# Optimization experiments

Hardware: AMD Instinct MI355X
Metric: run time of the kernel (lower is better)

## Reference

```python
import jax, jax.numpy as jnp
import numpy as np

NUM_SAMPLES = 9


def _resize1d(x, out_size, axis):
    """Bilinear (align_corners=False) resize along one axis, matching torch."""
    in_size = x.shape[axis]
    scale = in_size / out_size
    dst = jnp.arange(out_size, dtype=jnp.float32)
    src = jnp.maximum((dst + 0.5) * scale - 0.5, 0.0)
    i0 = jnp.floor(src).astype(jnp.int32)
    w1 = (src - i0).astype(x.dtype)
    i0 = jnp.clip(i0, 0, in_size - 1)
    i1 = jnp.clip(i0 + 1, 0, in_size - 1)
    x0 = jnp.take(x, i0, axis=axis)
    x1 = jnp.take(x, i1, axis=axis)
    wshape = [1] * x.ndim
    wshape[axis] = out_size
    w1 = w1.reshape(wshape)
    return x0 * (1.0 - w1) + x1 * w1


def _rel_to_abs(x, ns):
    # x: (b, h, l, ns+l-1) -> (b, h, l, ns) via the pad/reshape skew trick
    b, h, l, c = x.shape
    x = jnp.pad(x, ((0, 0), (0, 0), (0, 0), (0, 1)))
    x = x.reshape(b, h, l * (c + 1))
    x = jnp.pad(x, ((0, 0), (0, 0), (0, ns - 1)))
    x = x.reshape(b, h, l + 1, ns + l - 1)
    return x[:, :, :l, l - 1:]


def _relative_logits_1d(q, rel_k, ns):
    # q: (b, heads, x, y, d); rel_k: (y+ns-1, d)
    logits = jnp.einsum('bhxyd,rd->bhxyr', q, rel_k)
    b, h, x, y, r = logits.shape
    logits = logits.reshape(b, h * x, y, r)
    return _rel_to_abs(logits, ns)


def setup_inputs() -> dict:
    key = jax.random.key(0)
    k1, k2, k3 = jax.random.split(key, 3)
    B, heads, Hh, Ww, d = 16, 8, 64, 64, 64
    scale = d ** (-0.5)
    q = jax.random.normal(k1, (B, heads, Hh, Ww, d), dtype=jnp.float32)
    rel_height = jax.random.normal(k2, (Hh + NUM_SAMPLES - 1, d), dtype=jnp.float32) * scale
    rel_width = jax.random.normal(k3, (Ww + NUM_SAMPLES - 1, d), dtype=jnp.float32) * scale
    return {"q": q, "H": Hh, "W": Ww, "rel_height": rel_height, "rel_width": rel_width}


def reference(q, H, W, rel_height, rel_width):
    ns = NUM_SAMPLES
    heads = q.shape[1]
    # bilinear resize of learned tables along the positional axis
    # (the dim_head axis is resized to its own size -> identity)
    rel_w = _resize1d(rel_width, W + ns - 1, axis=0)
    rel_h = _resize1d(rel_height, H + ns - 1, axis=0)

    rel_logits_w = _relative_logits_1d(q, rel_w, ns)          # (b, heads*H, W, ns)
    qT = jnp.swapaxes(q, 2, 3)                                # (b, heads, W, H, d)
    rel_logits_h = _relative_logits_1d(qT, rel_h, ns)         # (b, heads*W, H, ns)

    # torch interpolates (b, ns, heads*W, H) -> (heads*H, W); separable bilinear
    rel_logits_h = _resize1d(rel_logits_h, heads * H, axis=1)
    rel_logits_h = _resize1d(rel_logits_h, W, axis=2)
    return rel_logits_w + rel_logits_h
```

## Files before the change

### kernel.cpp

```cpp
#include <hip/hip_runtime.h>
#include <stdint.h>

#define NS 9

typedef _Float16 f16x8 __attribute__((ext_vector_type(8)));
typedef float    f32x4 __attribute__((ext_vector_type(4)));

#define SBAR __builtin_amdgcn_sched_barrier(0)
#define WAIT_VM(N) do { SBAR; asm volatile("s_waitcnt vmcnt(" #N ")" ::: "memory"); SBAR; } while (0)
#define WAIT_LGKM0 do { SBAR; asm volatile("s_waitcnt lgkmcnt(0)" ::: "memory"); SBAR; } while (0)

__device__ __forceinline__ unsigned int pk(float a, float b) {
    return __builtin_bit_cast(unsigned int, __builtin_amdgcn_cvt_pkrtz(a, b));
}


__global__ __launch_bounds__(256, 2) void relpos_kernel(
    const float* __restrict__ q,
    const float* __restrict__ relh,
    const float* __restrict__ relw,
    float* __restrict__ out)
{
    __shared__ uint4 S1[16][16][8];
    __shared__ uint4 S2[16][16][8];
    __shared__ uint4 RL[2][2][32][8];

    const int bh  = blockIdx.x & 127;
    const int wid = blockIdx.x >> 7;
    const int ta  = wid < 4 ? 0 : wid < 7 ? 1 : wid < 9 ? 2 : 3;
    const int tc  = wid < 4 ? wid : wid < 7 ? wid - 3 : wid < 9 ? wid - 5 : 3;
    const int Ta0 = ta << 4, Tc0 = tc << 4;

    const int t    = threadIdx.x;
    const int lane = t & 63;
    const int wvu  = __builtin_amdgcn_readfirstlane(t >> 6);
    const int jl   = lane & 15;
    const int k4p  = lane >> 4;

    const float* __restrict__ qs = q + ((size_t)bh << 18);

    const int hrow = t >> 7;
    const int u    = t & 127;
    const int cc   = u >> 3;
    const int k4   = u & 7;

    float4 sA[16], sB[16], sR[6];
#pragma unroll
    for (int p = 0; p < 8; ++p) {
        const int a = 2 * p + hrow;
        const float* g1 = qs + (size_t)(Ta0 + a) * 4096 + (size_t)(Tc0 + cc) * 64 + k4 * 8;
        sA[2 * p]     = *(const float4*)g1;
        sA[2 * p + 1] = *(const float4*)(g1 + 4);
    }
    SBAR;
#pragma unroll
    for (int p = 0; p < 8; ++p) {
        const int a = 2 * p + hrow;
        const float* g2 = qs + (size_t)(Tc0 + a) * 4096 + (size_t)(Ta0 + cc) * 64 + k4 * 8;
        sB[2 * p]     = *(const float4*)g2;
        sB[2 * p + 1] = *(const float4*)(g2 + 4);
    }
    SBAR;
#pragma unroll
    for (int m = 0; m < 3; ++m) {
        int ch  = t + (m << 8);
        int win = ch >= 384;  int r = ch - (win ? 384 : 0);
        int tbl = r >= 192;   r -= (tbl ? 192 : 0);
        const int row = r >> 3, kk = r & 7;
        const int rb0 = win ? (48 - Ta0) : (48 - Tc0);
        const float* rp = (tbl ? relw : relh) + (size_t)(rb0 + row) * 64 + kk * 8;
        sR[2 * m]     = *(const float4*)rp;
        sR[2 * m + 1] = *(const float4*)(rp + 4);
    }
    SBAR;

    WAIT_VM(22);
#pragma unroll
    for (int p = 0; p < 8; ++p) {
        const int a = 2 * p + hrow;
        uint4 w;
        w.x = pk(sA[2 * p].x,     sA[2 * p].y);
        w.y = pk(sA[2 * p].z,     sA[2 * p].w);
        w.z = pk(sA[2 * p + 1].x, sA[2 * p + 1].y);
        w.w = pk(sA[2 * p + 1].z, sA[2 * p + 1].w);
        S1[a][cc][k4 ^ ((a ^ cc) & 7)] = w;
    }
    WAIT_VM(6);
#pragma unroll
    for (int p = 0; p < 8; ++p) {
        const int a = 2 * p + hrow;
        uint4 w;
        w.x = pk(sB[2 * p].x,     sB[2 * p].y);
        w.y = pk(sB[2 * p].z,     sB[2 * p].w);
        w.z = pk(sB[2 * p + 1].x, sB[2 * p + 1].y);
        w.w = pk(sB[2 * p + 1].z, sB[2 * p + 1].w);
        S2[a][cc][k4 ^ ((a ^ cc) & 7)] = w;
    }
    WAIT_VM(0);
#pragma unroll
    for (int m = 0; m < 3; ++m) {
        int ch  = t + (m << 8);
        int win = ch >= 384;  int r = ch - (win ? 384 : 0);
        int tbl = r >= 192;   r -= (tbl ? 192 : 0);
        const int row = r >> 3, kk = r & 7;
        uint4 w;
        w.x = pk(sR[2 * m].x,     sR[2 * m].y);
        w.y = pk(sR[2 * m].z,     sR[2 * m].w);
        w.z = pk(sR[2 * m + 1].x, sR[2 * m + 1].y);
        w.w = pk(sR[2 * m + 1].z, sR[2 * m + 1].w);
        RL[win][tbl][row][kk ^ (row & 7)] = w;
    }
    WAIT_LGKM0;
    __builtin_amdgcn_s_barrier();

    auto pass = [&](const uint4 (*P)[16][8], const uint4 (*Q)[16][8], int w,
                    int Arow0, int Ccol0) {
        uint4 ra[16], rb[16];
#pragma unroll
        for (int it = 0; it < 4; ++it) {
            const int cl = (wvu << 2) | it;
            const int sx = (jl ^ cl) & 7;
            ra[it * 4 + 0] = P[jl][cl][(k4p)     ^ sx];
            ra[it * 4 + 1] = P[jl][cl][(4 + k4p) ^ sx];
            ra[it * 4 + 2] = Q[cl][jl][(k4p)     ^ sx];
            ra[it * 4 + 3] = Q[cl][jl][(4 + k4p) ^ sx];
            const int rl = (15 - cl) + jl;
            rb[it * 4 + 0] = RL[w][1][rl][(k4p)     ^ (rl & 7)];
            rb[it * 4 + 1] = RL[w][1][rl][(4 + k4p) ^ (rl & 7)];
            rb[it * 4 + 2] = RL[w][0][rl][(k4p)     ^ (rl & 7)];
            rb[it * 4 + 3] = RL[w][0][rl][(4 + k4p) ^ (rl & 7)];
        }
        WAIT_LGKM0;

        f32x4 acc[4];
#pragma unroll
        for (int it = 0; it < 4; ++it) acc[it] = (f32x4){0.f, 0.f, 0.f, 0.f};
#pragma unroll
        for (int r = 0; r < 4; ++r)
#pragma unroll
            for (int it = 0; it < 4; ++it)
                acc[it] = __builtin_amdgcn_mfma_f32_16x16x32_f16(
                    __builtin_bit_cast(f16x8, ra[it * 4 + r]),
                    __builtin_bit_cast(f16x8, rb[it * 4 + r]),
                    acc[it], 0, 0, 0);

        if (jl < NS) {
            const int ar = k4p << 2;
            const size_t ob = (size_t)bh << 6;
#pragma unroll
            for (int it = 0; it < 4; ++it) {
                const int cl = (wvu << 2) | it;
#pragma unroll
                for (int r = 0; r < 4; ++r)
                    out[((ob + (Arow0 + ar + r)) * 64 + (Ccol0 + cl)) * NS + jl] = acc[it][r];
            }
        }
    };

    pass(S1, S2, 0, Ta0, Tc0);
    if (ta != tc)
        pass(S2, S1, 1, Tc0, Ta0);
}

extern "C" void kernel_launch(void* const* d_in, const int* in_sizes, int n_in,
                              void* d_out, int out_size, void* d_ws, size_t ws_size,
                              hipStream_t stream) {
    const float* q    = (const float*)d_in[0];
    const float* relh = (const float*)d_in[3];
    const float* relw = (const float*)d_in[4];
    float* out = (float*)d_out;

    relpos_kernel<<<dim3(1280), dim3(256), 0, stream>>>(q, relh, relw, out);
}
```

Before: 37.17 us.

## Process two batch-heads per block, prefetching the second during first compute

Each block now handles two (batch,head) slices, so the grid is halved to 640 blocks. The global loads for the second slice are issued into registers while the first slice's MFMA passes run, overlapping memory latency with compute. The rel-table loads are amortised across both slices. The pass also interleaves LDS reads with MFMAs using partial lgkmcnt waits instead of loading all operands first. The cost is fewer blocks for latency hiding and a serial dependency inside each block.

```diff
diff --git a/kernel.cpp b/kernel.cpp
--- a/kernel.cpp
+++ b/kernel.cpp
@@ -8,7 +8,7 @@
 
 #define SBAR __builtin_amdgcn_sched_barrier(0)
 #define WAIT_VM(N) do { SBAR; asm volatile("s_waitcnt vmcnt(" #N ")" ::: "memory"); SBAR; } while (0)
-#define WAIT_LGKM0 do { SBAR; asm volatile("s_waitcnt lgkmcnt(0)" ::: "memory"); SBAR; } while (0)
+#define WAIT_LGKM(N) do { SBAR; asm volatile("s_waitcnt lgkmcnt(" #N ")" ::: "memory"); SBAR; } while (0)
 
 __device__ __forceinline__ unsigned int pk(float a, float b) {
     return __builtin_bit_cast(unsigned int, __builtin_amdgcn_cvt_pkrtz(a, b));
@@ -25,8 +25,10 @@
     __shared__ uint4 S2[16][16][8];
     __shared__ uint4 RL[2][2][32][8];
 
-    const int bh  = blockIdx.x & 127;
-    const int wid = blockIdx.x >> 7;
+    const int blk = blockIdx.x;
+    const int wid = blk >> 6;
+    const int m   = blk & 63;
+    const int bh0 = m << 1, bh1 = bh0 | 1;
     const int ta  = wid < 4 ? 0 : wid < 7 ? 1 : wid < 9 ? 2 : 3;
     const int tc  = wid < 4 ? wid : wid < 7 ? wid - 3 : wid < 9 ? wid - 5 : 3;
     const int Ta0 = ta << 4, Tc0 = tc << 4;
@@ -37,116 +39,117 @@
     const int jl   = lane & 15;
     const int k4p  = lane >> 4;
 
-    const float* __restrict__ qs = q + ((size_t)bh << 18);
-
     const int hrow = t >> 7;
     const int u    = t & 127;
     const int cc   = u >> 3;
     const int k4   = u & 7;
 
     float4 sA[16], sB[16], sR[6];
+
+    auto issueS = [&](int bh_) {
+        const float* qs = q + ((size_t)bh_ << 18);
 #pragma unroll
-    for (int p = 0; p < 8; ++p) {
-        const int a = 2 * p + hrow;
-        const float* g1 = qs + (size_t)(Ta0 + a) * 4096 + (size_t)(Tc0 + cc) * 64 + k4 * 8;
-        sA[2 * p]     = *(const float4*)g1;
-        sA[2 * p + 1] = *(const float4*)(g1 + 4);
-    }
-    SBAR;
+        for (int p = 0; p < 8; ++p) {
+            const int a = 2 * p + hrow;
+            const float* g1 = qs + (size_t)(Ta0 + a) * 4096 + (size_t)(Tc0 + cc) * 64 + k4 * 8;
+            sA[2 * p]     = *(const float4*)g1;
+            sA[2 * p + 1] = *(const float4*)(g1 + 4);
+        }
+        SBAR;
 #pragma unroll
-    for (int p = 0; p < 8; ++p) {
-        const int a = 2 * p + hrow;
-        const float* g2 = qs + (size_t)(Tc0 + a) * 4096 + (size_t)(Ta0 + cc) * 64 + k4 * 8;
-        sB[2 * p]     = *(const float4*)g2;
-        sB[2 * p + 1] = *(const float4*)(g2 + 4);
-    }
-    SBAR;
+        for (int p = 0; p < 8; ++p) {
+            const int a = 2 * p + hrow;
+            const float* g2 = qs + (size_t)(Tc0 + a) * 4096 + (size_t)(Ta0 + cc) * 64 + k4 * 8;
+            sB[2 * p]     = *(const float4*)g2;
+            sB[2 * p + 1] = *(const float4*)(g2 + 4);
+        }
+        SBAR;
+    };
+    auto writeS = [&]() {
 #pragma unroll
-    for (int m = 0; m < 3; ++m) {
-        int ch  = t + (m << 8);
+        for (int p = 0; p < 8; ++p) {
+            const int a = 2 * p + hrow;
+            uint4 w;
+            w.x = pk(sA[2 * p].x,     sA[2 * p].y);
+            w.y = pk(sA[2 * p].z,     sA[2 * p].w);
+            w.z = pk(sA[2 * p + 1].x, sA[2 * p + 1].y);
+            w.w = pk(sA[2 * p + 1].z, sA[2 * p + 1].w);
+            S1[a][cc][k4 ^ ((a ^ cc) & 7)] = w;
+        }
+#pragma unroll
+        for (int p = 0; p < 8; ++p) {
+            const int a = 2 * p + hrow;
+            uint4 w;
+            w.x = pk(sB[2 * p].x,     sB[2 * p].y);
+            w.y = pk(sB[2 * p].z,     sB[2 * p].w);
+            w.z = pk(sB[2 * p + 1].x, sB[2 * p + 1].y);
+            w.w = pk(sB[2 * p + 1].z, sB[2 * p + 1].w);
+            S2[a][cc][k4 ^ ((a ^ cc) & 7)] = w;
+        }
+    };
+
+#pragma unroll
+    for (int mm = 0; mm < 3; ++mm) {
+        int ch  = t + (mm << 8);
         int win = ch >= 384;  int r = ch - (win ? 384 : 0);
         int tbl = r >= 192;   r -= (tbl ? 192 : 0);
         const int row = r >> 3, kk = r & 7;
         const int rb0 = win ? (48 - Ta0) : (48 - Tc0);
         const float* rp = (tbl ? relw : relh) + (size_t)(rb0 + row) * 64 + kk * 8;
-        sR[2 * m]     = *(const float4*)rp;
-        sR[2 * m + 1] = *(const float4*)(rp + 4);
+        sR[2 * mm]     = *(const float4*)rp;
+        sR[2 * mm + 1] = *(const float4*)(rp + 4);
     }
     SBAR;
+    issueS(bh0);
 
-    WAIT_VM(22);
+    WAIT_VM(32);
 #pragma unroll
-    for (int p = 0; p < 8; ++p) {
-        const int a = 2 * p + hrow;
-        uint4 w;
-        w.x = pk(sA[2 * p].x,     sA[2 * p].y);
-        w.y = pk(sA[2 * p].z,     sA[2 * p].w);
-        w.z = pk(sA[2 * p + 1].x, sA[2 * p + 1].y);
-        w.w = pk(sA[2 * p + 1].z, sA[2 * p + 1].w);
-        S1[a][cc][k4 ^ ((a ^ cc) & 7)] = w;
-    }
-    WAIT_VM(6);
-#pragma unroll
-    for (int p = 0; p < 8; ++p) {
-        const int a = 2 * p + hrow;
-        uint4 w;
-        w.x = pk(sB[2 * p].x,     sB[2 * p].y);
-        w.y = pk(sB[2 * p].z,     sB[2 * p].w);
-        w.z = pk(sB[2 * p + 1].x, sB[2 * p + 1].y);
-        w.w = pk(sB[2 * p + 1].z, sB[2 * p + 1].w);
-        S2[a][cc][k4 ^ ((a ^ cc) & 7)] = w;
-    }
-    WAIT_VM(0);
-#pragma unroll
-    for (int m = 0; m < 3; ++m) {
-        int ch  = t + (m << 8);
+    for (int mm = 0; mm < 3; ++mm) {
+        int ch  = t + (mm << 8);
         int win = ch >= 384;  int r = ch - (win ? 384 : 0);
         int tbl = r >= 192;   r -= (tbl ? 192 : 0);
         const int row = r >> 3, kk = r & 7;
         uint4 w;
-        w.x = pk(sR[2 * m].x,     sR[2 * m].y);
-        w.y = pk(sR[2 * m].z,     sR[2 * m].w);
-        w.z = pk(sR[2 * m + 1].x, sR[2 * m + 1].y);
-        w.w = pk(sR[2 * m + 1].z, sR[2 * m + 1].w);
+        w.x = pk(sR[2 * mm].x,     sR[2 * mm].y);
+        w.y = pk(sR[2 * mm].z,     sR[2 * mm].w);
+        w.z = pk(sR[2 * mm + 1].x, sR[2 * mm + 1].y);
+        w.w = pk(sR[2 * mm + 1].z, sR[2 * mm + 1].w);
         RL[win][tbl][row][kk ^ (row & 7)] = w;
     }
-    WAIT_LGKM0;
-    __builtin_amdgcn_s_barrier();
 
     auto pass = [&](const uint4 (*P)[16][8], const uint4 (*Q)[16][8], int w,
-                    int Arow0, int Ccol0) {
-        uint4 ra[16], rb[16];
+                    int Arow0, int Ccol0, size_t ob) {
+        uint4 a0[4], b0[4], a1[4], b1[4];
+        auto RD = [&](int r, uint4* A, uint4* B) {
+            const int kh = (r & 1) << 2;
 #pragma unroll
-        for (int it = 0; it < 4; ++it) {
-            const int cl = (wvu << 2) | it;
-            const int sx = (jl ^ cl) & 7;
-            ra[it * 4 + 0] = P[jl][cl][(k4p)     ^ sx];
-            ra[it * 4 + 1] = P[jl][cl][(4 + k4p) ^ sx];
-            ra[it * 4 + 2] = Q[cl][jl][(k4p)     ^ sx];
-            ra[it * 4 + 3] = Q[cl][jl][(4 + k4p) ^ sx];
-            const int rl = (15 - cl) + jl;
-            rb[it * 4 + 0] = RL[w][1][rl][(k4p)     ^ (rl & 7)];
-            rb[it * 4 + 1] = RL[w][1][rl][(4 + k4p) ^ (rl & 7)];
-            rb[it * 4 + 2] = RL[w][0][rl][(k4p)     ^ (rl & 7)];
-            rb[it * 4 + 3] = RL[w][0][rl][(4 + k4p) ^ (rl & 7)];
-        }
-        WAIT_LGKM0;
-
+            for (int it = 0; it < 4; ++it) {
+                const int cl = (wvu << 2) | it;
+                const int sx = (jl ^ cl) & 7;
+                A[it] = (r < 2) ? P[jl][cl][(kh + k4p) ^ sx]
+                                : Q[cl][jl][(kh + k4p) ^ sx];
+                const int rl = (15 - cl) + jl;
+                B[it] = RL[w][r < 2 ? 1 : 0][rl][(kh + k4p) ^ (rl & 7)];
+            }
+        };
         f32x4 acc[4];
 #pragma unroll
         for (int it = 0; it < 4; ++it) acc[it] = (f32x4){0.f, 0.f, 0.f, 0.f};
-#pragma unroll
-        for (int r = 0; r < 4; ++r)
+        auto MF = [&](const uint4* A, const uint4* B) {
 #pragma unroll
             for (int it = 0; it < 4; ++it)
                 acc[it] = __builtin_amdgcn_mfma_f32_16x16x32_f16(
-                    __builtin_bit_cast(f16x8, ra[it * 4 + r]),
-                    __builtin_bit_cast(f16x8, rb[it * 4 + r]),
-                    acc[it], 0, 0, 0);
+                    __builtin_bit_cast(f16x8, A[it]),
+                    __builtin_bit_cast(f16x8, B[it]), acc[it], 0, 0, 0);
+        };
+        RD(0, a0, b0); RD(1, a1, b1);
+        WAIT_LGKM(8);  MF(a0, b0);  RD(2, a0, b0);
+        WAIT_LGKM(8);  MF(a1, b1);  RD(3, a1, b1);
+        WAIT_LGKM(8);  MF(a0, b0);
+        WAIT_LGKM(0);  MF(a1, b1);
 
         if (jl < NS) {
             const int ar = k4p << 2;
-            const size_t ob = (size_t)bh << 6;
 #pragma unroll
             for (int it = 0; it < 4; ++it) {
                 const int cl = (wvu << 2) | it;
@@ -157,9 +160,27 @@
         }
     };
 
-    pass(S1, S2, 0, Ta0, Tc0);
-    if (ta != tc)
-        pass(S2, S1, 1, Tc0, Ta0);
+    WAIT_VM(0);
+    writeS();
+    issueS(bh1);
+    WAIT_LGKM(0);
+    __builtin_amdgcn_s_barrier();
+    {
+        const size_t ob = (size_t)bh0 << 6;
+        pass(S1, S2, 0, Ta0, Tc0, ob);
+        if (ta != tc) pass(S2, S1, 1, Tc0, Ta0, ob);
+    }
+    __builtin_amdgcn_s_barrier();
+
+    WAIT_VM(0);
+    writeS();
+    WAIT_LGKM(0);
+    __builtin_amdgcn_s_barrier();
+    {
+        const size_t ob = (size_t)bh1 << 6;
+        pass(S1, S2, 0, Ta0, Tc0, ob);
+        if (ta != tc) pass(S2, S1, 1, Tc0, Ta0, ob);
+    }
 }
 
 extern "C" void kernel_launch(void* const* d_in, const int* in_sizes, int n_in,
@@ -170,5 +191,5 @@
     const float* relw = (const float*)d_in[4];
     float* out = (float*)d_out;
 
-    relpos_kernel<<<dim3(1280), dim3(256), 0, stream>>>(q, relh, relw, out);
+    relpos_kernel<<<dim3(640), dim3(256), 0, stream>>>(q, relh, relw, out);
 }
```

Measured after the change: 45.98 us. 1.24x slower.

## Double block threads so two wave groups run both tile passes in parallel

Applied to the files above, without the earlier changes.

Blocks grow from 256 to 512 threads. The two symmetric tile passes that were run one after the other are now given to two groups of four waves, which lets them run at the same time. Global loads are remapped so each thread loads half as many float4s and writes uint2 halves into the swizzled LDS tiles. The LDS operand reads are split into k-chunks that are double-buffered with partial lgkmcnt waits, so MFMAs overlap the remaining reads. On diagonal tiles the second wave group does no work, and the larger block raises register and occupancy pressure.

```diff
diff --git a/kernel.cpp b/kernel.cpp
--- a/kernel.cpp
+++ b/kernel.cpp
@@ -8,14 +8,14 @@
 
 #define SBAR __builtin_amdgcn_sched_barrier(0)
 #define WAIT_VM(N) do { SBAR; asm volatile("s_waitcnt vmcnt(" #N ")" ::: "memory"); SBAR; } while (0)
-#define WAIT_LGKM0 do { SBAR; asm volatile("s_waitcnt lgkmcnt(0)" ::: "memory"); SBAR; } while (0)
+#define WAIT_LGKM(N) do { SBAR; asm volatile("s_waitcnt lgkmcnt(" #N ")" ::: "memory"); SBAR; } while (0)
 
 __device__ __forceinline__ unsigned int pk(float a, float b) {
     return __builtin_bit_cast(unsigned int, __builtin_amdgcn_cvt_pkrtz(a, b));
 }
 
 
-__global__ __launch_bounds__(256, 2) void relpos_kernel(
+__global__ __launch_bounds__(512, 4) void relpos_kernel(
     const float* __restrict__ q,
     const float* __restrict__ relh,
     const float* __restrict__ relw,
@@ -25,8 +25,9 @@
     __shared__ uint4 S2[16][16][8];
     __shared__ uint4 RL[2][2][32][8];
 
-    const int bh  = blockIdx.x & 127;
-    const int wid = blockIdx.x >> 7;
+    const int blk = blockIdx.x;
+    const int bh  = blk & 127;
+    const int wid = blk >> 7;
     const int ta  = wid < 4 ? 0 : wid < 7 ? 1 : wid < 9 ? 2 : 3;
     const int tc  = wid < 4 ? wid : wid < 7 ? wid - 3 : wid < 9 ? wid - 5 : 3;
     const int Ta0 = ta << 4, Tc0 = tc << 4;
@@ -34,132 +35,126 @@
     const int t    = threadIdx.x;
     const int lane = t & 63;
     const int wvu  = __builtin_amdgcn_readfirstlane(t >> 6);
+    const int wg   = wvu >> 2;
+    const int wl   = wvu & 3;
     const int jl   = lane & 15;
     const int k4p  = lane >> 4;
 
     const float* __restrict__ qs = q + ((size_t)bh << 18);
 
-    const int hrow = t >> 7;
-    const int u    = t & 127;
-    const int cc   = u >> 3;
-    const int k4   = u & 7;
-
-    float4 sA[16], sB[16], sR[6];
+    float4 sA[8], sB[8], sR[3];
 #pragma unroll
-    for (int p = 0; p < 8; ++p) {
-        const int a = 2 * p + hrow;
-        const float* g1 = qs + (size_t)(Ta0 + a) * 4096 + (size_t)(Tc0 + cc) * 64 + k4 * 8;
-        sA[2 * p]     = *(const float4*)g1;
-        sA[2 * p + 1] = *(const float4*)(g1 + 4);
+    for (int i = 0; i < 8; ++i) {
+        const int F  = (i << 9) + t;
+        const int al = F >> 8, cc = (F >> 4) & 15, g = F & 15;
+        sA[i] = *(const float4*)(qs + (size_t)(Ta0 + al) * 4096
+                                    + (size_t)(Tc0 + cc) * 64 + (g << 2));
     }
     SBAR;
 #pragma unroll
-    for (int p = 0; p < 8; ++p) {
-        const int a = 2 * p + hrow;
-        const float* g2 = qs + (size_t)(Tc0 + a) * 4096 + (size_t)(Ta0 + cc) * 64 + k4 * 8;
-        sB[2 * p]     = *(const float4*)g2;
-        sB[2 * p + 1] = *(const float4*)(g2 + 4);
+    for (int i = 0; i < 8; ++i) {
+        const int F  = (i << 9) + t;
+        const int al = F >> 8, cc = (F >> 4) & 15, g = F & 15;
+        sB[i] = *(const float4*)(qs + (size_t)(Tc0 + al) * 4096
+                                    + (size_t)(Ta0 + cc) * 64 + (g << 2));
     }
     SBAR;
 #pragma unroll
     for (int m = 0; m < 3; ++m) {
-        int ch  = t + (m << 8);
-        int win = ch >= 384;  int r = ch - (win ? 384 : 0);
-        int tbl = r >= 192;   r -= (tbl ? 192 : 0);
-        const int row = r >> 3, kk = r & 7;
+        const int F   = (m << 9) + t;
+        const int win = F >= 768;
+        const int r   = F - (win ? 768 : 0);
+        const int tbl = r >= 384;
+        const int rr  = r - (tbl ? 384 : 0);
+        const int row = rr >> 4, g = rr & 15;
         const int rb0 = win ? (48 - Ta0) : (48 - Tc0);
-        const float* rp = (tbl ? relw : relh) + (size_t)(rb0 + row) * 64 + kk * 8;
-        sR[2 * m]     = *(const float4*)rp;
-        sR[2 * m + 1] = *(const float4*)(rp + 4);
+        int gr = rb0 + row; if (gr > 71) gr = 71;
+        sR[m] = *(const float4*)((tbl ? relw : relh) + (size_t)gr * 64 + (g << 2));
     }
     SBAR;
 
-    WAIT_VM(22);
+    WAIT_VM(11);
 #pragma unroll
-    for (int p = 0; p < 8; ++p) {
-        const int a = 2 * p + hrow;
-        uint4 w;
-        w.x = pk(sA[2 * p].x,     sA[2 * p].y);
-        w.y = pk(sA[2 * p].z,     sA[2 * p].w);
-        w.z = pk(sA[2 * p + 1].x, sA[2 * p + 1].y);
-        w.w = pk(sA[2 * p + 1].z, sA[2 * p + 1].w);
-        S1[a][cc][k4 ^ ((a ^ cc) & 7)] = w;
+    for (int i = 0; i < 8; ++i) {
+        const int F  = (i << 9) + t;
+        const int al = F >> 8, cc = (F >> 4) & 15, g = F & 15;
+        const int slot = (g >> 1) ^ ((al ^ cc) & 7), half = g & 1;
+        uint2 w; w.x = pk(sA[i].x, sA[i].y); w.y = pk(sA[i].z, sA[i].w);
+        ((uint2*)&S1[al][cc][slot])[half] = w;
     }
-    WAIT_VM(6);
+    WAIT_VM(3);
 #pragma unroll
-    for (int p = 0; p < 8; ++p) {
-        const int a = 2 * p + hrow;
-        uint4 w;
-        w.x = pk(sB[2 * p].x,     sB[2 * p].y);
-        w.y = pk(sB[2 * p].z,     sB[2 * p].w);
-        w.z = pk(sB[2 * p + 1].x, sB[2 * p + 1].y);
-        w.w = pk(sB[2 * p + 1].z, sB[2 * p + 1].w);
-        S2[a][cc][k4 ^ ((a ^ cc) & 7)] = w;
+    for (int i = 0; i < 8; ++i) {
+        const int F  = (i << 9) + t;
+        const int al = F >> 8, cc = (F >> 4) & 15, g = F & 15;
+        const int slot = (g >> 1) ^ ((al ^ cc) & 7), half = g & 1;
+        uint2 w; w.x = pk(sB[i].x, sB[i].y); w.y = pk(sB[i].z, sB[i].w);
+        ((uint2*)&S2[al][cc][slot])[half] = w;
     }
     WAIT_VM(0);
 #pragma unroll
     for (int m = 0; m < 3; ++m) {
-        int ch  = t + (m << 8);
-        int win = ch >= 384;  int r = ch - (win ? 384 : 0);
-        int tbl = r >= 192;   r -= (tbl ? 192 : 0);
-        const int row = r >> 3, kk = r & 7;
-        uint4 w;
-        w.x = pk(sR[2 * m].x,     sR[2 * m].y);
-        w.y = pk(sR[2 * m].z,     sR[2 * m].w);
-        w.z = pk(sR[2 * m + 1].x, sR[2 * m + 1].y);
-        w.w = pk(sR[2 * m + 1].z, sR[2 * m + 1].w);
-        RL[win][tbl][row][kk ^ (row & 7)] = w;
+        const int F   = (m << 9) + t;
+        const int win = F >= 768;
+        const int r   = F - (win ? 768 : 0);
+        const int tbl = r >= 384;
+        const int rr  = r - (tbl ? 384 : 0);
+        const int row = rr >> 4, g = rr & 15;
+        const int slot = (g >> 1) ^ (row & 7), half = g & 1;
+        uint2 w; w.x = pk(sR[m].x, sR[m].y); w.y = pk(sR[m].z, sR[m].w);
+        ((uint2*)&RL[win][tbl][row][slot])[half] = w;
     }
-    WAIT_LGKM0;
+    WAIT_LGKM(0);
     __builtin_amdgcn_s_barrier();
 
-    auto pass = [&](const uint4 (*P)[16][8], const uint4 (*Q)[16][8], int w,
-                    int Arow0, int Ccol0) {
-        uint4 ra[16], rb[16];
+    if (wg == 0 || ta != tc) {
+        const uint4 (*P)[16][8] = wg ? S2 : S1;
+        const uint4 (*Q)[16][8] = wg ? S1 : S2;
+        const int win   = wg;
+        const int Arow0 = wg ? Tc0 : Ta0;
+        const int Ccol0 = wg ? Ta0 : Tc0;
+
+        uint4 A0[4], B0[4], A1[4], B1[4];
+        auto RD = [&](int r, uint4* A, uint4* B) {
+            const int kh = (r & 1) << 2;
 #pragma unroll
-        for (int it = 0; it < 4; ++it) {
-            const int cl = (wvu << 2) | it;
-            const int sx = (jl ^ cl) & 7;
-            ra[it * 4 + 0] = P[jl][cl][(k4p)     ^ sx];
-            ra[it * 4 + 1] = P[jl][cl][(4 + k4p) ^ sx];
-            ra[it * 4 + 2] = Q[cl][jl][(k4p)     ^ sx];
-            ra[it * 4 + 3] = Q[cl][jl][(4 + k4p) ^ sx];
-            const int rl = (15 - cl) + jl;
-            rb[it * 4 + 0] = RL[w][1][rl][(k4p)     ^ (rl & 7)];
-            rb[it * 4 + 1] = RL[w][1][rl][(4 + k4p) ^ (rl & 7)];
-            rb[it * 4 + 2] = RL[w][0][rl][(k4p)     ^ (rl & 7)];
-            rb[it * 4 + 3] = RL[w][0][rl][(4 + k4p) ^ (rl & 7)];
-        }
-        WAIT_LGKM0;
-
+            for (int it = 0; it < 4; ++it) {
+                const int cl = (wl << 2) | it;
+                const int sx = (jl ^ cl) & 7;
+                A[it] = (r < 2) ? P[jl][cl][(kh + k4p) ^ sx]
+                                : Q[cl][jl][(kh + k4p) ^ sx];
+                const int rl = (15 - cl) + jl;
+                B[it] = RL[win][r < 2 ? 1 : 0][rl][(kh + k4p) ^ (rl & 7)];
+            }
+        };
         f32x4 acc[4];
 #pragma unroll
         for (int it = 0; it < 4; ++it) acc[it] = (f32x4){0.f, 0.f, 0.f, 0.f};
-#pragma unroll
-        for (int r = 0; r < 4; ++r)
+        auto MF = [&](const uint4* A, const uint4* B) {
 #pragma unroll
             for (int it = 0; it < 4; ++it)
                 acc[it] = __builtin_amdgcn_mfma_f32_16x16x32_f16(
-                    __builtin_bit_cast(f16x8, ra[it * 4 + r]),
-                    __builtin_bit_cast(f16x8, rb[it * 4 + r]),
-                    acc[it], 0, 0, 0);
+                    __builtin_bit_cast(f16x8, A[it]),
+                    __builtin_bit_cast(f16x8, B[it]), acc[it], 0, 0, 0);
+        };
+        RD(0, A0, B0); RD(1, A1, B1);
+        WAIT_LGKM(8);  MF(A0, B0);  RD(2, A0, B0);
+        WAIT_LGKM(8);  MF(A1, B1);  RD(3, A1, B1);
+        WAIT_LGKM(8);  MF(A0, B0);
+        WAIT_LGKM(0);  MF(A1, B1);
 
         if (jl < NS) {
             const int ar = k4p << 2;
             const size_t ob = (size_t)bh << 6;
 #pragma unroll
             for (int it = 0; it < 4; ++it) {
-                const int cl = (wvu << 2) | it;
+                const int cl = (wl << 2) | it;
 #pragma unroll
                 for (int r = 0; r < 4; ++r)
                     out[((ob + (Arow0 + ar + r)) * 64 + (Ccol0 + cl)) * NS + jl] = acc[it][r];
             }
         }
-    };
-
-    pass(S1, S2, 0, Ta0, Tc0);
-    if (ta != tc)
-        pass(S2, S1, 1, Tc0, Ta0);
+    }
 }
 
 extern "C" void kernel_launch(void* const* d_in, const int* in_sizes, int n_in,
@@ -170,5 +165,5 @@
     const float* relw = (const float*)d_in[4];
     float* out = (float*)d_out;
 
-    relpos_kernel<<<dim3(1280), dim3(256), 0, stream>>>(q, relh, relw, out);
+    relpos_kernel<<<dim3(1280), dim3(512), 0, stream>>>(q, relh, relw, out);
 }
```

Measured after the change: 31.19 us. 1.19x faster.
